# Performance work log

Hardware: AMD Instinct MI355X
Metric: run time of the kernel (lower is better)

## Reference

```python
import jax, jax.numpy as jnp
import numpy as np

N, E, D, H, C, G = 80000, 1280000, 64, 64, 5, 512


def setup_inputs() -> dict:
    key = jax.random.key(0)
    ks = jax.random.split(key, 8)
    h = jax.random.normal(ks[0], (N, D), jnp.float32)
    src = jax.random.randint(ks[1], (E,), 0, N)
    dst = jax.random.randint(ks[2], (E,), 0, N)
    graph_ids = jnp.sort(jax.random.randint(ks[3], (N,), 0, G))
    # Glorot-ish init for weights
    W1 = jax.random.normal(ks[4], (D, H), jnp.float32) * (1.0 / np.sqrt(D))
    b1 = jnp.zeros((H,), jnp.float32)
    W2 = jax.random.normal(ks[5], (H, H), jnp.float32) * (1.0 / np.sqrt(H))
    b2 = jnp.zeros((H,), jnp.float32)
    Wc = jax.random.normal(ks[6], (H, C), jnp.float32) * (1.0 / np.sqrt(H))
    bc = jnp.zeros((C,), jnp.float32)
    return dict(h=h, src=src, dst=dst, graph_ids=graph_ids,
                W1=W1, b1=b1, W2=W2, b2=b2, Wc=Wc, bc=bc, num_graphs=G)


def reference(h, src, dst, graph_ids, W1, b1, W2, b2, Wc, bc, num_graphs):
    n = h.shape[0]
    ones_e = jnp.ones(src.shape[0], h.dtype)
    # DGL GraphConv norm='both': symmetric normalization, degrees clamped to >=1
    out_deg = jnp.clip(jax.ops.segment_sum(ones_e, src, num_segments=n), 1.0)
    in_deg = jnp.clip(jax.ops.segment_sum(ones_e, dst, num_segments=n), 1.0)
    norm_src = jax.lax.rsqrt(out_deg)  # [N]
    norm_dst = jax.lax.rsqrt(in_deg)   # [N]

    def graph_conv(x, W, b):
        x = x * norm_src[:, None]                                   # scale by D_out^{-1/2}
        agg = jax.ops.segment_sum(x[src], dst, num_segments=n)      # sparse A^T x (copy_u + sum)
        agg = agg * norm_dst[:, None]                               # scale by D_in^{-1/2}
        return agg @ W + b

    h1 = jax.nn.relu(graph_conv(h, W1, b1))
    h2 = jax.nn.relu(graph_conv(h1, W2, b2))

    # dgl.mean_nodes: per-graph mean pooling over nodes
    cnt = jnp.clip(jax.ops.segment_sum(jnp.ones(n, h.dtype), graph_ids,
                                       num_segments=num_graphs), 1.0)
    hg = jax.ops.segment_sum(h2, graph_ids, num_segments=num_graphs) / cnt[:, None]
    return hg @ Wc + bc  # [G, C] logits
```

## Files before the change

kernel.cpp:

```cpp
#include <hip/hip_runtime.h>
#include <hip/hip_bf16.h>


#define NBK 160
#define HB  256

typedef __attribute__((ext_vector_type(8))) short bf16x8;
typedef __attribute__((ext_vector_type(4))) float f32x4;

__device__ __forceinline__ float bflo(unsigned u) { return __uint_as_float(u << 16); }
__device__ __forceinline__ float bfhi(unsigned u) { return __uint_as_float(u & 0xffff0000u); }
__device__ __forceinline__ float bf1(unsigned short u) { return __uint_as_float((unsigned)u << 16); }
__device__ __forceinline__ unsigned short f2bf(float f) {
    unsigned u = __float_as_uint(f);
    return (unsigned short)((u + 0x7fff + ((u >> 16) & 1)) >> 16);
}
__device__ __forceinline__ unsigned packbf(float lo, float hi) {
    return (unsigned)f2bf(lo) | ((unsigned)f2bf(hi) << 16);
}

__global__ __launch_bounds__(256) void p1_hist(
    const int* __restrict__ src, const int* __restrict__ dst,
    int* __restrict__ histD, int* __restrict__ histS,
    const int* __restrict__ gids, int* __restrict__ goffs,
    int E, int NB, int N, int G)
{
    if (blockIdx.x >= HB) {
        int i = (blockIdx.x - HB) * 256 + threadIdx.x;
        if (i >= N) return;
        int b = gids[i];
        if (i == 0) {
            for (int g = 0; g <= b; g++) goffs[g] = 0;
        } else {
            int a = gids[i - 1];
            for (int g = a + 1; g <= b; g++) goffs[g] = i;
        }
        if (i == N - 1) {
            for (int g = b + 1; g <= G; g++) goffs[g] = N;
        }
        return;
    }
    __shared__ int hd[NBK], hs[NBK];
    for (int i = threadIdx.x; i < NB; i += 256) { hd[i] = 0; hs[i] = 0; }
    __syncthreads();
    int chunk = (E + HB - 1) / HB;
    int s0 = blockIdx.x * chunk, s1 = min(E, s0 + chunk);
    for (int i = s0 + threadIdx.x; i < s1; i += 256) {
        atomicAdd(&hd[dst[i] >> 9], 1);
        atomicAdd(&hs[src[i] >> 9], 1);
    }
    __syncthreads();
    for (int b = threadIdx.x; b < NB; b += 256) {
        histD[b * 256 + blockIdx.x] = hd[b];
        histS[b * 256 + blockIdx.x] = hs[b];
    }
}

__global__ __launch_bounds__(256) void p2_scanblocks(
    int* __restrict__ histD, int* __restrict__ histS,
    int* __restrict__ btotD, int* __restrict__ btotS, int NB)
{
    int b = blockIdx.x;
    bool dmode = b < NB;
    int* h = dmode ? (histD + b * 256) : (histS + (b - NB) * 256);
    int t = threadIdx.x, lane = t & 63, w = t >> 6;
    int v = h[t];
    int x = v;
    #pragma unroll
    for (int off = 1; off < 64; off <<= 1) {
        int y = __shfl_up(x, off);
        if (lane >= off) x += y;
    }
    __shared__ int wt[4];
    if (lane == 63) wt[w] = x;
    __syncthreads();
    int bw = 0;
    for (int i = 0; i < w; i++) bw += wt[i];
    h[t] = x - v + bw;
    if (t == 255) (dmode ? btotD : btotS)[dmode ? b : b - NB] = x + bw;
}

__global__ __launch_bounds__(256) void p3_scanbuckets(
    const int* __restrict__ btotD, const int* __restrict__ btotS,
    int* __restrict__ baseD, int* __restrict__ baseS,
    int* __restrict__ row_offs, int E, int NB, int N)
{
    __shared__ int wt[4];
    int t = threadIdx.x, lane = t & 63, w = t >> 6;
    int v = (t < NB) ? btotD[t] : 0;
    int x = v;
    #pragma unroll
    for (int off = 1; off < 64; off <<= 1) {
        int y = __shfl_up(x, off);
        if (lane >= off) x += y;
    }
    if (lane == 63) wt[w] = x;
    __syncthreads();
    int bw = 0;
    for (int i = 0; i < w; i++) bw += wt[i];
    if (t <= NB) baseD[t] = x - v + bw;
    __syncthreads();
    v = (t < NB) ? btotS[t] : 0;
    x = v;
    #pragma unroll
    for (int off = 1; off < 64; off <<= 1) {
        int y = __shfl_up(x, off);
        if (lane >= off) x += y;
    }
    if (lane == 63) wt[w] = x;
    __syncthreads();
    bw = 0;
    for (int i = 0; i < w; i++) bw += wt[i];
    if (t <= NB) baseS[t] = x - v + bw;
    if (t == 0) row_offs[N] = E;
}

__global__ __launch_bounds__(256) void p4_scatter(
    const int* __restrict__ src, const int* __restrict__ dst,
    const int* __restrict__ histD, const int* __restrict__ histS,
    const int* __restrict__ baseD, const int* __restrict__ baseS,
    int* __restrict__ pack, unsigned short* __restrict__ sloc, int E, int NB)
{
    __shared__ int cd[NBK], cs[NBK];
    for (int b = threadIdx.x; b < NB; b += 256) {
        cd[b] = baseD[b] + histD[b * 256 + blockIdx.x];
        cs[b] = baseS[b] + histS[b * 256 + blockIdx.x];
    }
    __syncthreads();
    int chunk = (E + gridDim.x - 1) / gridDim.x;
    int s0 = blockIdx.x * chunk, s1 = min(E, s0 + chunk);
    for (int i = s0 + threadIdx.x; i < s1; i += 256) {
        int s = src[i], d = dst[i];
        int pd = atomicAdd(&cd[d >> 9], 1);
        pack[pd] = ((d & 511) << 17) | s;
        int ps = atomicAdd(&cs[s >> 9], 1);
        sloc[ps] = (unsigned short)(s & 511);
    }
}

__global__ __launch_bounds__(256) void p5_build(
    const int* __restrict__ pack, const unsigned short* __restrict__ sloc,
    const int* __restrict__ baseD, const int* __restrict__ baseS,
    int* __restrict__ col, int* __restrict__ row_offs,
    float* __restrict__ nsrc, float* __restrict__ ndst,
    const float* __restrict__ h, unsigned short* __restrict__ xs,
    int N, int NB)
{
    __shared__ int hist[512];
    __shared__ float nsl[512];
    __shared__ int wt[4];
    int t = threadIdx.x;
    bool dmode = blockIdx.x < NB;
    int b = dmode ? blockIdx.x : blockIdx.x - NB;
    int n0 = b << 9, n1 = min(N, n0 + 512);
    hist[t] = 0; hist[t + 256] = 0;
    __syncthreads();
    int e0 = dmode ? baseD[b] : baseS[b];
    int e1 = dmode ? baseD[b + 1] : baseS[b + 1];
    if (!dmode) {
        for (int i = e0 + t; i < e1; i += 256)
            atomicAdd(&hist[sloc[i]], 1);
        __syncthreads();
        for (int n = n0 + t; n < n1; n += 256) {
            float s = rsqrtf((float)max(hist[n - n0], 1));
            nsrc[n] = s;
            nsl[n - n0] = s;
        }
        __syncthreads();
        int cnt = n1 - n0;
        const float2* h2p = (const float2*)h;
        ushort2* xp = (ushort2*)xs;
        for (int i = t; i < cnt * 32; i += 256) {
            int node = i >> 5;
            float s = nsl[node];
            float2 v = h2p[(size_t)(n0 + node) * 32 + (i & 31)];
            ushort2 o;
            o.x = f2bf(v.x * s);
            o.y = f2bf(v.y * s);
            xp[(size_t)(n0 + node) * 32 + (i & 31)] = o;
        }
        return;
    }
    for (int i = e0 + t; i < e1; i += 256)
        atomicAdd(&hist[pack[i] >> 17], 1);
    __syncthreads();
    int c0 = hist[2 * t], c1 = hist[2 * t + 1];
    int v = c0 + c1;
    int lane = t & 63, w = t >> 6;
    int x = v;
    #pragma unroll
    for (int off = 1; off < 64; off <<= 1) {
        int y = __shfl_up(x, off);
        if (lane >= off) x += y;
    }
    if (lane == 63) wt[w] = x;
    __syncthreads();
    int bw = 0;
    for (int i = 0; i < w; i++) bw += wt[i];
    int excl = x - v + bw;
    int n = n0 + 2 * t;
    if (n < n1) {
        row_offs[n] = e0 + excl;
        ndst[n] = rsqrtf((float)max(c0, 1));
    }
    if (n + 1 < n1) {
        row_offs[n + 1] = e0 + excl + c0;
        ndst[n + 1] = rsqrtf((float)max(c1, 1));
    }
    hist[2 * t] = excl;
    hist[2 * t + 1] = excl + c0;
    __syncthreads();
    for (int i = e0 + t; i < e1; i += 256) {
        int wd = pack[i];
        int pos = atomicAdd(&hist[wd >> 17], 1);
        col[e0 + pos] = wd & 0x1FFFF;
    }
}

__global__ __launch_bounds__(256) void agg_kernel(
    const unsigned short* __restrict__ z, unsigned short* __restrict__ y,
    const int* __restrict__ col, const int* __restrict__ row_offs, int N)
{
    int lane = threadIdx.x & 63;
    int sub  = lane >> 3;
    int li   = lane & 7;
    const uint4* x4 = (const uint4*)z;

    int wid = (blockIdx.x * 256 + threadIdx.x) >> 6;
    int nw  = (gridDim.x * 256) >> 6;
    for (int node = wid; node < N; node += nw) {
        int ro0 = row_offs[node];
        int cnt = row_offs[node + 1] - ro0;
        float a0=0.f,a1=0.f,a2=0.f,a3=0.f,a4=0.f,a5=0.f,a6=0.f,a7=0.f;
        for (int c0 = 0; c0 < cnt; c0 += 64) {
            int m = min(cnt - c0, 64);
            int idx = 0;
            if (lane < m) idx = col[ro0 + c0 + lane];
            for (int i = 0; i < m; i += 32) {
                int e1 = i + sub, e2 = i + 8 + sub, e3 = i + 16 + sub, e4 = i + 24 + sub;
                int s1 = __shfl(idx, min(e1, m - 1));
                int s2 = __shfl(idx, min(e2, m - 1));
                int s3 = __shfl(idx, min(e3, m - 1));
                int s4 = __shfl(idx, min(e4, m - 1));
                uint4 v1 = make_uint4(0u,0u,0u,0u), v2 = make_uint4(0u,0u,0u,0u);
                uint4 v3 = make_uint4(0u,0u,0u,0u), v4 = make_uint4(0u,0u,0u,0u);
                if (e1 < m) v1 = x4[(size_t)s1 * 8 + li];
                if (e2 < m) v2 = x4[(size_t)s2 * 8 + li];
                if (e3 < m) v3 = x4[(size_t)s3 * 8 + li];
                if (e4 < m) v4 = x4[(size_t)s4 * 8 + li];
                a0 += bflo(v1.x); a1 += bfhi(v1.x);
                a2 += bflo(v1.y); a3 += bfhi(v1.y);
                a4 += bflo(v1.z); a5 += bfhi(v1.z);
                a6 += bflo(v1.w); a7 += bfhi(v1.w);
                a0 += bflo(v2.x); a1 += bfhi(v2.x);
                a2 += bflo(v2.y); a3 += bfhi(v2.y);
                a4 += bflo(v2.z); a5 += bfhi(v2.z);
                a6 += bflo(v2.w); a7 += bfhi(v2.w);
                a0 += bflo(v3.x); a1 += bfhi(v3.x);
                a2 += bflo(v3.y); a3 += bfhi(v3.y);
                a4 += bflo(v3.z); a5 += bfhi(v3.z);
                a6 += bflo(v3.w); a7 += bfhi(v3.w);
                a0 += bflo(v4.x); a1 += bfhi(v4.x);
                a2 += bflo(v4.y); a3 += bfhi(v4.y);
                a4 += bflo(v4.z); a5 += bfhi(v4.z);
                a6 += bflo(v4.w); a7 += bfhi(v4.w);
            }
        }
        #pragma unroll
        for (int off = 8; off <= 32; off <<= 1) {
            a0 += __shfl_xor(a0, off); a1 += __shfl_xor(a1, off);
            a2 += __shfl_xor(a2, off); a3 += __shfl_xor(a3, off);
            a4 += __shfl_xor(a4, off); a5 += __shfl_xor(a5, off);
            a6 += __shfl_xor(a6, off); a7 += __shfl_xor(a7, off);
        }
        if (sub == 0) {
            uint4 o;
            o.x = packbf(a0, a1);
            o.y = packbf(a2, a3);
            o.z = packbf(a4, a5);
            o.w = packbf(a6, a7);
            ((uint4*)y)[(size_t)node * 8 + li] = o;
        }
    }
}

__global__ __launch_bounds__(256) void gemm_kernel(
    const unsigned short* __restrict__ A, const float* __restrict__ W,
    const float* __restrict__ b, const float* __restrict__ ndst,
    const float* __restrict__ nsrc, unsigned short* __restrict__ Z,
    int M, int scale_out)
{
    int t = threadIdx.x, lane = t & 63, w = t >> 6;
    int col = lane & 15, quad = lane >> 4;
    bf16x8 bfrag[4][2];
    #pragma unroll
    for (int nt = 0; nt < 4; nt++)
        #pragma unroll
        for (int ks = 0; ks < 2; ks++)
            #pragma unroll
            for (int j = 0; j < 8; j++)
                bfrag[nt][ks][j] =
                    (short)f2bf(W[(ks * 32 + quad * 8 + j) * 64 + nt * 16 + col]);
    float bias[4];
    #pragma unroll
    for (int nt = 0; nt < 4; nt++) bias[nt] = b[nt * 16 + col];

    int mbase = blockIdx.x * 64 + w * 16;
    if (mbase >= M) return;
    int row = min(mbase + col, M - 1);
    const uint4* a4 = (const uint4*)A;
    union { uint4 u; bf16x8 v; } a0, a1;
    a0.u = a4[(size_t)row * 8 + quad];
    a1.u = a4[(size_t)row * 8 + 4 + quad];

    float nd[4], ns[4];
    #pragma unroll
    for (int r = 0; r < 4; r++) {
        int m = min(mbase + quad * 4 + r, M - 1);
        nd[r] = ndst[m];
        ns[r] = scale_out ? nsrc[m] : 1.f;
    }

    #pragma unroll
    for (int nt = 0; nt < 4; nt++) {
        f32x4 acc = {0.f, 0.f, 0.f, 0.f};
        acc = __builtin_amdgcn_mfma_f32_16x16x32_bf16(a0.v, bfrag[nt][0], acc, 0, 0, 0);
        acc = __builtin_amdgcn_mfma_f32_16x16x32_bf16(a1.v, bfrag[nt][1], acc, 0, 0, 0);
        #pragma unroll
        for (int r = 0; r < 4; r++) {
            int m = mbase + quad * 4 + r;
            if (m < M)
                Z[(size_t)m * 64 + nt * 16 + col] =
                    f2bf(fmaxf(nd[r] * acc[r] + bias[nt], 0.f) * ns[r]);
        }
    }
}

__global__ __launch_bounds__(256) void pool_kernel(
    const unsigned short* __restrict__ h2, const int* __restrict__ goffs,
    const float* __restrict__ Wc, const float* __restrict__ bc,
    float* __restrict__ out)
{
    int g = blockIdx.x;
    int lane = threadIdx.x & 63;
    int w = threadIdx.x >> 6;
    int s = goffs[g], e = goffs[g + 1];
    float acc = 0.f;
    for (int i = s + w; i < e; i += 4) acc += bf1(h2[i * 64 + lane]);
    __shared__ float red[4][64];
    red[w][lane] = acc;
    __syncthreads();
    if (w == 0) {
        float tot = red[0][lane] + red[1][lane] + red[2][lane] + red[3][lane];
        float mean = tot / (float)max(e - s, 1);
        float wc[5];
        #pragma unroll
        for (int c = 0; c < 5; c++) wc[c] = Wc[lane * 5 + c];
        #pragma unroll
        for (int c = 0; c < 5; c++) {
            float p = mean * wc[c];
            #pragma unroll
            for (int off = 32; off; off >>= 1) p += __shfl_down(p, off);
            if (lane == 0) out[g * 5 + c] = p + bc[c];
        }
    }
}

extern "C" void kernel_launch(void* const* d_in, const int* in_sizes, int n_in,
                              void* d_out, int out_size, void* d_ws, size_t ws_size,
                              hipStream_t stream)
{
    const float* h    = (const float*)d_in[0];
    const int*   src  = (const int*)d_in[1];
    const int*   dst  = (const int*)d_in[2];
    const int*   gids = (const int*)d_in[3];
    const float* W1   = (const float*)d_in[4];
    const float* b1   = (const float*)d_in[5];
    const float* W2   = (const float*)d_in[6];
    const float* b2   = (const float*)d_in[7];
    const float* Wc   = (const float*)d_in[8];
    const float* bc   = (const float*)d_in[9];
    float* out = (float*)d_out;

    const int N = in_sizes[0] / 64;
    const int E = in_sizes[1];
    const int G = out_size / 5;
    const int NB = (N + 511) >> 9;
    const int NBB = (N + 255) / 256;

    auto align = [](size_t x) { return (x + 255) & ~(size_t)255; };
    char* p = (char*)d_ws;
    int* histD   = (int*)p;            p += align((size_t)NBK * 256 * 4);
    int* histS   = (int*)p;            p += align((size_t)NBK * 256 * 4);
    int* btotD   = (int*)p;            p += align((size_t)NBK * 4);
    int* btotS   = (int*)p;            p += align((size_t)NBK * 4);
    int* baseD   = (int*)p;            p += align((size_t)(NBK + 1) * 4);
    int* baseS   = (int*)p;            p += align((size_t)(NBK + 1) * 4);
    int* row_offs= (int*)p;            p += align((size_t)(N + 1) * 4);
    float* nsrc  = (float*)p;          p += align((size_t)N * 4);
    float* ndst  = (float*)p;          p += align((size_t)N * 4);
    int* goffs   = (int*)p;            p += align((size_t)(G + 1) * 4);
    int* pack    = (int*)p;            p += align((size_t)E * 4);
    unsigned short* sloc = (unsigned short*)p; p += align((size_t)E * 2);
    int* col     = (int*)p;            p += align((size_t)E * 4);
    unsigned short* xs  = (unsigned short*)p; p += align((size_t)N * 64 * 2);
    unsigned short* s1  = (unsigned short*)p; p += align((size_t)N * 64 * 2);
    unsigned short* h1s = (unsigned short*)p; p += align((size_t)N * 64 * 2);
    unsigned short* s2  = s1;
    unsigned short* h2  = xs;

    p1_hist<<<HB + NBB, 256, 0, stream>>>(src, dst, histD, histS,
                                          gids, goffs, E, NB, N, G);
    p2_scanblocks<<<2 * NB, 256, 0, stream>>>(histD, histS, btotD, btotS, NB);
    p3_scanbuckets<<<1, 256, 0, stream>>>(btotD, btotS, baseD, baseS,
                                          row_offs, E, NB, N);
    p4_scatter<<<256, 256, 0, stream>>>(src, dst, histD, histS, baseD, baseS,
                                        pack, sloc, E, NB);
    p5_build<<<2 * NB, 256, 0, stream>>>(pack, sloc, baseD, baseS, col,
                                         row_offs, nsrc, ndst, h, xs, N, NB);

    agg_kernel<<<2048, 256, 0, stream>>>(xs, s1, col, row_offs, N);
    gemm_kernel<<<(N + 63) / 64, 256, 0, stream>>>(s1, W1, b1, ndst, nsrc,
                                                   h1s, N, 1);
    agg_kernel<<<2048, 256, 0, stream>>>(h1s, s2, col, row_offs, N);
    gemm_kernel<<<(N + 63) / 64, 256, 0, stream>>>(s2, W2, b2, ndst, nsrc,
                                                   h2, N, 0);

    pool_kernel<<<G, 256, 0, stream>>>(h2, goffs, Wc, bc, out);
}
```

Measured before the change: 238.4 us.

## Fuse sparse aggregation with MFMA GEMM into a single per-layer kernel

Merges the gather-sum aggregation and the dense 64x64 GEMM into one layer kernel. Each block aggregates 64 destination rows into an LDS tile, then runs MFMA on that tile directly, which removes the intermediate bf16 buffer round trip through global memory and one launch per layer. A wave now processes four nodes at once, with a fast path when every degree is at most 32 and a butterfly shuffle that reduces all four nodes together. The grid shrinks from a fixed persistent 2048 blocks to one block per 64 nodes, which changes load balance, and the extra registers may lower occupancy.

```diff
diff --git a/kernel.cpp b/kernel.cpp
--- a/kernel.cpp
+++ b/kernel.cpp
@@ -217,81 +217,20 @@
     }
 }
 
-__global__ __launch_bounds__(256) void agg_kernel(
-    const unsigned short* __restrict__ z, unsigned short* __restrict__ y,
-    const int* __restrict__ col, const int* __restrict__ row_offs, int N)
-{
-    int lane = threadIdx.x & 63;
-    int sub  = lane >> 3;
-    int li   = lane & 7;
-    const uint4* x4 = (const uint4*)z;
-
-    int wid = (blockIdx.x * 256 + threadIdx.x) >> 6;
-    int nw  = (gridDim.x * 256) >> 6;
-    for (int node = wid; node < N; node += nw) {
-        int ro0 = row_offs[node];
-        int cnt = row_offs[node + 1] - ro0;
-        float a0=0.f,a1=0.f,a2=0.f,a3=0.f,a4=0.f,a5=0.f,a6=0.f,a7=0.f;
-        for (int c0 = 0; c0 < cnt; c0 += 64) {
-            int m = min(cnt - c0, 64);
-            int idx = 0;
-            if (lane < m) idx = col[ro0 + c0 + lane];
-            for (int i = 0; i < m; i += 32) {
-                int e1 = i + sub, e2 = i + 8 + sub, e3 = i + 16 + sub, e4 = i + 24 + sub;
-                int s1 = __shfl(idx, min(e1, m - 1));
-                int s2 = __shfl(idx, min(e2, m - 1));
-                int s3 = __shfl(idx, min(e3, m - 1));
-                int s4 = __shfl(idx, min(e4, m - 1));
-                uint4 v1 = make_uint4(0u,0u,0u,0u), v2 = make_uint4(0u,0u,0u,0u);
-                uint4 v3 = make_uint4(0u,0u,0u,0u), v4 = make_uint4(0u,0u,0u,0u);
-                if (e1 < m) v1 = x4[(size_t)s1 * 8 + li];
-                if (e2 < m) v2 = x4[(size_t)s2 * 8 + li];
-                if (e3 < m) v3 = x4[(size_t)s3 * 8 + li];
-                if (e4 < m) v4 = x4[(size_t)s4 * 8 + li];
-                a0 += bflo(v1.x); a1 += bfhi(v1.x);
-                a2 += bflo(v1.y); a3 += bfhi(v1.y);
-                a4 += bflo(v1.z); a5 += bfhi(v1.z);
-                a6 += bflo(v1.w); a7 += bfhi(v1.w);
-                a0 += bflo(v2.x); a1 += bfhi(v2.x);
-                a2 += bflo(v2.y); a3 += bfhi(v2.y);
-                a4 += bflo(v2.z); a5 += bfhi(v2.z);
-                a6 += bflo(v2.w); a7 += bfhi(v2.w);
-                a0 += bflo(v3.x); a1 += bfhi(v3.x);
-                a2 += bflo(v3.y); a3 += bfhi(v3.y);
-                a4 += bflo(v3.z); a5 += bfhi(v3.z);
-                a6 += bflo(v3.w); a7 += bfhi(v3.w);
-                a0 += bflo(v4.x); a1 += bfhi(v4.x);
-                a2 += bflo(v4.y); a3 += bfhi(v4.y);
-                a4 += bflo(v4.z); a5 += bfhi(v4.z);
-                a6 += bflo(v4.w); a7 += bfhi(v4.w);
-            }
-        }
-        #pragma unroll
-        for (int off = 8; off <= 32; off <<= 1) {
-            a0 += __shfl_xor(a0, off); a1 += __shfl_xor(a1, off);
-            a2 += __shfl_xor(a2, off); a3 += __shfl_xor(a3, off);
-            a4 += __shfl_xor(a4, off); a5 += __shfl_xor(a5, off);
-            a6 += __shfl_xor(a6, off); a7 += __shfl_xor(a7, off);
-        }
-        if (sub == 0) {
-            uint4 o;
-            o.x = packbf(a0, a1);
-            o.y = packbf(a2, a3);
-            o.z = packbf(a4, a5);
-            o.w = packbf(a6, a7);
-            ((uint4*)y)[(size_t)node * 8 + li] = o;
-        }
-    }
-}
-
-__global__ __launch_bounds__(256) void gemm_kernel(
-    const unsigned short* __restrict__ A, const float* __restrict__ W,
-    const float* __restrict__ b, const float* __restrict__ ndst,
-    const float* __restrict__ nsrc, unsigned short* __restrict__ Z,
-    int M, int scale_out)
-{
+__global__ __launch_bounds__(256) void layer_kernel(
+    const unsigned short* __restrict__ x,
+    const int* __restrict__ col, const int* __restrict__ row_offs,
+    const float* __restrict__ W, const float* __restrict__ b,
+    const float* __restrict__ ndst, const float* __restrict__ nsrc,
+    unsigned short* __restrict__ y,
+    int N, int scale_out)
+{
+    __shared__ __align__(16) unsigned short As[64][72];
     int t = threadIdx.x, lane = t & 63, w = t >> 6;
-    int col = lane & 15, quad = lane >> 4;
+    int sub = lane >> 3, li = lane & 7;
+    int c16 = lane & 15, quad = lane >> 4;
+    const uint4* x4 = (const uint4*)x;
+
     bf16x8 bfrag[4][2];
     #pragma unroll
     for (int nt = 0; nt < 4; nt++)
@@ -300,38 +239,133 @@
             #pragma unroll
             for (int j = 0; j < 8; j++)
                 bfrag[nt][ks][j] =
-                    (short)f2bf(W[(ks * 32 + quad * 8 + j) * 64 + nt * 16 + col]);
+                    (short)f2bf(W[(ks * 32 + quad * 8 + j) * 64 + nt * 16 + c16]);
     float bias[4];
     #pragma unroll
-    for (int nt = 0; nt < 4; nt++) bias[nt] = b[nt * 16 + col];
-
-    int mbase = blockIdx.x * 64 + w * 16;
-    if (mbase >= M) return;
-    int row = min(mbase + col, M - 1);
-    const uint4* a4 = (const uint4*)A;
+    for (int nt = 0; nt < 4; nt++) bias[nt] = b[nt * 16 + c16];
+
+    int nblk = blockIdx.x * 64;
+
+    #pragma unroll 1
+    for (int r = 0; r < 4; r++) {
+        int nb = nblk + w * 16 + r * 4;
+        int rv = 0;
+        if (lane < 5) rv = row_offs[min(nb + lane, N)];
+        int ro[4], cn[4];
+        #pragma unroll
+        for (int j = 0; j < 4; j++) {
+            ro[j] = __shfl(rv, j);
+            int nxt = __shfl(rv, j + 1);
+            cn[j] = (nb + j < N) ? (nxt - ro[j]) : 0;
+        }
+        int idx0 = 0, idx1 = 0, idx2 = 0, idx3 = 0;
+        if (lane < cn[0]) idx0 = col[ro[0] + lane];
+        if (lane < cn[1]) idx1 = col[ro[1] + lane];
+        if (lane < cn[2]) idx2 = col[ro[2] + lane];
+        if (lane < cn[3]) idx3 = col[ro[3] + lane];
+
+        float A[4][8];
+        #pragma unroll
+        for (int j = 0; j < 4; j++)
+            #pragma unroll
+            for (int k = 0; k < 8; k++) A[j][k] = 0.f;
+
+        bool fast = (cn[0] <= 32) & (cn[1] <= 32) & (cn[2] <= 32) & (cn[3] <= 32);
+        if (fast) {
+            #pragma unroll
+            for (int j = 0; j < 4; j++) {
+                int idx = j == 0 ? idx0 : j == 1 ? idx1 : j == 2 ? idx2 : idx3;
+                int c = cn[j];
+                int cm = max(c - 1, 0);
+                int e0 = sub, e1 = 8 + sub, e2 = 16 + sub, e3 = 24 + sub;
+                int s0 = __shfl(idx, min(e0, cm));
+                int s1 = __shfl(idx, min(e1, cm));
+                int s2 = __shfl(idx, min(e2, cm));
+                int s3 = __shfl(idx, min(e3, cm));
+                uint4 v0 = make_uint4(0u,0u,0u,0u), v1 = v0, v2 = v0, v3 = v0;
+                if (e0 < c) v0 = x4[(size_t)s0 * 8 + li];
+                if (e1 < c) v1 = x4[(size_t)s1 * 8 + li];
+                if (e2 < c) v2 = x4[(size_t)s2 * 8 + li];
+                if (e3 < c) v3 = x4[(size_t)s3 * 8 + li];
+                A[j][0] += bflo(v0.x) + bflo(v1.x) + bflo(v2.x) + bflo(v3.x);
+                A[j][1] += bfhi(v0.x) + bfhi(v1.x) + bfhi(v2.x) + bfhi(v3.x);
+                A[j][2] += bflo(v0.y) + bflo(v1.y) + bflo(v2.y) + bflo(v3.y);
+                A[j][3] += bfhi(v0.y) + bfhi(v1.y) + bfhi(v2.y) + bfhi(v3.y);
+                A[j][4] += bflo(v0.z) + bflo(v1.z) + bflo(v2.z) + bflo(v3.z);
+                A[j][5] += bfhi(v0.z) + bfhi(v1.z) + bfhi(v2.z) + bfhi(v3.z);
+                A[j][6] += bflo(v0.w) + bflo(v1.w) + bflo(v2.w) + bflo(v3.w);
+                A[j][7] += bfhi(v0.w) + bfhi(v1.w) + bfhi(v2.w) + bfhi(v3.w);
+            }
+        } else {
+            #pragma unroll
+            for (int j = 0; j < 4; j++) {
+                int idx = j == 0 ? idx0 : j == 1 ? idx1 : j == 2 ? idx2 : idx3;
+                int c = cn[j], roj = ro[j];
+                for (int cc = 0; cc < c; cc += 64) {
+                    int m = min(c - cc, 64);
+                    if (cc > 0) idx = (lane < m) ? col[roj + cc + lane] : 0;
+                    for (int i = 0; i < m; i += 8) {
+                        int e = i + sub;
+                        int s = __shfl(idx, min(e, m - 1));
+                        if (e < m) {
+                            uint4 v = x4[(size_t)s * 8 + li];
+                            A[j][0] += bflo(v.x); A[j][1] += bfhi(v.x);
+                            A[j][2] += bflo(v.y); A[j][3] += bfhi(v.y);
+                            A[j][4] += bflo(v.z); A[j][5] += bfhi(v.z);
+                            A[j][6] += bflo(v.w); A[j][7] += bfhi(v.w);
+                        }
+                    }
+                }
+            }
+        }
+        bool o1 = (sub & 1), o2 = (sub & 2);
+        float D[8];
+        #pragma unroll
+        for (int k = 0; k < 8; k++) {
+            float u0 = __shfl_xor(A[0][k], 8);
+            float u1 = __shfl_xor(A[1][k], 8);
+            float u2 = __shfl_xor(A[2][k], 8);
+            float u3 = __shfl_xor(A[3][k], 8);
+            float b0 = o1 ? (A[1][k] + u1) : (A[0][k] + u0);
+            float b1 = o1 ? (A[3][k] + u3) : (A[2][k] + u2);
+            float v0 = __shfl_xor(b0, 16);
+            float v1 = __shfl_xor(b1, 16);
+            float c  = o2 ? (b1 + v1) : (b0 + v0);
+            D[k] = c + __shfl_xor(c, 32);
+        }
+        if (sub < 4) {
+            int rowi = w * 16 + r * 4 + sub;
+            uint4 o;
+            o.x = packbf(D[0], D[1]);
+            o.y = packbf(D[2], D[3]);
+            o.z = packbf(D[4], D[5]);
+            o.w = packbf(D[6], D[7]);
+            *(uint4*)&As[rowi][li * 8] = o;
+        }
+    }
+    __syncthreads();
+
     union { uint4 u; bf16x8 v; } a0, a1;
-    a0.u = a4[(size_t)row * 8 + quad];
-    a1.u = a4[(size_t)row * 8 + 4 + quad];
-
+    a0.u = *(const uint4*)&As[w * 16 + c16][quad * 8];
+    a1.u = *(const uint4*)&As[w * 16 + c16][32 + quad * 8];
     float nd[4], ns[4];
     #pragma unroll
-    for (int r = 0; r < 4; r++) {
-        int m = min(mbase + quad * 4 + r, M - 1);
-        nd[r] = ndst[m];
-        ns[r] = scale_out ? nsrc[m] : 1.f;
-    }
-
+    for (int rr = 0; rr < 4; rr++) {
+        int m = min(nblk + w * 16 + quad * 4 + rr, N - 1);
+        nd[rr] = ndst[m];
+        ns[rr] = scale_out ? nsrc[m] : 1.f;
+    }
     #pragma unroll
     for (int nt = 0; nt < 4; nt++) {
         f32x4 acc = {0.f, 0.f, 0.f, 0.f};
         acc = __builtin_amdgcn_mfma_f32_16x16x32_bf16(a0.v, bfrag[nt][0], acc, 0, 0, 0);
         acc = __builtin_amdgcn_mfma_f32_16x16x32_bf16(a1.v, bfrag[nt][1], acc, 0, 0, 0);
         #pragma unroll
-        for (int r = 0; r < 4; r++) {
-            int m = mbase + quad * 4 + r;
-            if (m < M)
-                Z[(size_t)m * 64 + nt * 16 + col] =
-                    f2bf(fmaxf(nd[r] * acc[r] + bias[nt], 0.f) * ns[r]);
+        for (int rr = 0; rr < 4; rr++) {
+            int m = nblk + w * 16 + quad * 4 + rr;
+            if (m < N)
+                y[(size_t)m * 64 + nt * 16 + c16] =
+                    f2bf(fmaxf(nd[rr] * acc[rr] + bias[nt], 0.f) * ns[rr]);
         }
     }
 }
@@ -404,9 +438,7 @@
     unsigned short* sloc = (unsigned short*)p; p += align((size_t)E * 2);
     int* col     = (int*)p;            p += align((size_t)E * 4);
     unsigned short* xs  = (unsigned short*)p; p += align((size_t)N * 64 * 2);
-    unsigned short* s1  = (unsigned short*)p; p += align((size_t)N * 64 * 2);
     unsigned short* h1s = (unsigned short*)p; p += align((size_t)N * 64 * 2);
-    unsigned short* s2  = s1;
     unsigned short* h2  = xs;
 
     p1_hist<<<HB + NBB, 256, 0, stream>>>(src, dst, histD, histS,
@@ -419,12 +451,10 @@
     p5_build<<<2 * NB, 256, 0, stream>>>(pack, sloc, baseD, baseS, col,
                                          row_offs, nsrc, ndst, h, xs, N, NB);
 
-    agg_kernel<<<2048, 256, 0, stream>>>(xs, s1, col, row_offs, N);
-    gemm_kernel<<<(N + 63) / 64, 256, 0, stream>>>(s1, W1, b1, ndst, nsrc,
-                                                   h1s, N, 1);
-    agg_kernel<<<2048, 256, 0, stream>>>(h1s, s2, col, row_offs, N);
-    gemm_kernel<<<(N + 63) / 64, 256, 0, stream>>>(s2, W2, b2, ndst, nsrc,
-                                                   h2, N, 0);
+    layer_kernel<<<(N + 63) / 64, 256, 0, stream>>>(
+        xs, col, row_offs, W1, b1, ndst, nsrc, h1s, N, 1);
+    layer_kernel<<<(N + 63) / 64, 256, 0, stream>>>(
+        h1s, col, row_offs, W2, b2, ndst, nsrc, h2, N, 0);
 
     pool_kernel<<<G, 256, 0, stream>>>(h2, goffs, Wc, bc, out);
 }
```

New measurement: 250.7 us. 5.2% more time.
